# Performance work log

Hardware: AMD Instinct MI355X
Metric: run time of the kernel (lower is better)

The kernel has to match this reference:

```python
import jax, jax.numpy as jnp
import numpy as np

B, N, D_MODEL, H, BLK = 2, 2048, 1024, 16, 128
TB = N // BLK  # 16 blocks per side
NEG = -1e30


def setup_inputs() -> dict:
    key = jax.random.key(0)
    kq, kk, kv, kb = jax.random.split(key, 4)
    q = jax.random.normal(kq, (B, N, D_MODEL), jnp.float32)
    k = jax.random.normal(kk, (B, N, D_MODEL), jnp.float32)
    v = jax.random.normal(kv, (B, N, D_MODEL), jnp.float32)
    tau = jnp.float32(1.0)
    mask = jnp.ones((B, 1, N, N), jnp.int32)
    block_sparse_mask = jax.random.randint(kb, (TB, TB), 0, 2).astype(jnp.int32)
    return {"q": q, "k": k, "v": v, "tau": tau, "mask": mask,
            "block_sparse_mask": block_sparse_mask}


def reference(q, k, v, tau, mask, block_sparse_mask):
    # Equivalent closed form of the tiled online-softmax loop (dropout p=0, eval
    # mode): processed blocks accumulate exactly masked softmax(tau*QK^T/sqrt(dk))@V;
    # rows whose every block is skipped keep O=0, l=0, m=-inf.
    Bq, Nq, D = q.shape
    d_k = D // H
    qh = q.reshape(Bq, Nq, H, d_k).transpose(0, 2, 1, 3)  # (B,H,N,dk)
    kh = k.reshape(Bq, Nq, H, d_k).transpose(0, 2, 1, 3)
    vh = v.reshape(Bq, Nq, H, d_k).transpose(0, 2, 1, 3)

    S = tau * jnp.einsum('bhqd,bhkd->bhqk', qh, kh) / np.sqrt(d_k).astype(np.float32)

    # expand block-sparse pattern to token resolution (N,N)
    bs = jnp.repeat(jnp.repeat(block_sparse_mask, BLK, axis=0), BLK, axis=1)
    allowed = (mask != 0) & (bs != 0)  # (B,1,N,N), broadcasts over heads

    S_m = jnp.where(allowed, S, NEG)
    m = jnp.max(S_m, axis=-1, keepdims=True)            # (B,H,N,1)
    P = jnp.exp(S_m - m) * allowed.astype(S.dtype)      # masked exp-weights
    l = jnp.sum(P, axis=-1, keepdims=True)              # (B,H,N,1)
    Ov = jnp.einsum('bhqk,bhkd->bhqd', P, vh)
    O = Ov / jnp.where(l > 0, l, 1.0)

    has_any = jnp.any(allowed, axis=-1, keepdims=True)  # (B,1,N,1)
    m_out = jnp.where(has_any, m, -jnp.inf)
    O_out = O.transpose(0, 2, 1, 3).reshape(Bq, Nq, D)
    return O_out, l, m_out
```

## Files before the change

### kernel.cpp

```cpp
#include <hip/hip_runtime.h>
#include <hip/hip_bf16.h>

#define B_   2
#define N_   2048
#define DM_  1024
#define H_   16
#define DK_  64
#define BLK_ 128
#define TB_  16

typedef unsigned short u16;
typedef unsigned int   u32;
using bf16x8 = __attribute__((ext_vector_type(8))) __bf16;
using f32x4  = __attribute__((ext_vector_type(4))) float;

#define KPAD 72
#define VPAD 136
#define PPAD 136
#define OPAD 68
#define QROWS 64

__device__ __forceinline__ u32 pack_bf16(float a, float b) {
  __hip_bfloat162 h = __float22bfloat162_rn(make_float2(a, b));
  u32 u; __builtin_memcpy(&u, &h, 4); return u;
}
__device__ __forceinline__ bf16x8 pack8(float4 f0, float4 f1, float sc) {
  u32 w[4];
  w[0] = pack_bf16(f0.x * sc, f0.y * sc); w[1] = pack_bf16(f0.z * sc, f0.w * sc);
  w[2] = pack_bf16(f1.x * sc, f1.y * sc); w[3] = pack_bf16(f1.z * sc, f1.w * sc);
  bf16x8 r; __builtin_memcpy(&r, w, 16); return r;
}

__global__ void kv_convert(const float* __restrict__ k, const float* __restrict__ v,
                           u16* __restrict__ kb, u16* __restrict__ vt) {
  __shared__ u16 tile[BLK_][DK_ + 2];
  const int b = blockIdx.z, h = blockIdx.y, nb = blockIdx.x;
  const int t = threadIdx.x;
  const int rr = t >> 4, cc = (t & 15) * 4;
  {
    const float* kg = k + ((size_t)(b * N_ + nb * BLK_)) * DM_ + h * DK_;
    u16* kd = kb + ((size_t)((b * H_ + h) * N_) + nb * BLK_) * DK_;
#pragma unroll
    for (int i = 0; i < 8; ++i) {
      const int r = rr + i * 16;
      const float4 f = *(const float4*)(kg + (size_t)r * DM_ + cc);
      *(uint2*)(kd + r * DK_ + cc) = make_uint2(pack_bf16(f.x, f.y), pack_bf16(f.z, f.w));
    }
  }
  {
    const float* vg = v + ((size_t)(b * N_ + nb * BLK_)) * DM_ + h * DK_;
#pragma unroll
    for (int i = 0; i < 8; ++i) {
      const int r = rr + i * 16;
      const float4 f = *(const float4*)(vg + (size_t)r * DM_ + cc);
      *(u32*)(&tile[r][cc])     = pack_bf16(f.x, f.y);
      *(u32*)(&tile[r][cc + 2]) = pack_bf16(f.z, f.w);
    }
    __syncthreads();
    const int d = t & 63, n0 = (t >> 6) * 32;
    u16* og = vt + ((size_t)(b * H_ + h) * DK_ + d) * N_ + nb * BLK_ + n0;
#pragma unroll
    for (int j = 0; j < 32; j += 8) {
      u16 tmp[8];
#pragma unroll
      for (int x = 0; x < 8; ++x) tmp[x] = tile[n0 + j + x][d];
      uint4 w; __builtin_memcpy(&w, tmp, 16);
      *(uint4*)(og + j) = w;
    }
  }
}

__global__ void mask_flags_kernel(const int* __restrict__ mask, const int* __restrict__ bs,
                                  int* __restrict__ flags) {
  const int blk = blockIdx.x;
  const int kb = blk % TB_, qb = (blk / TB_) % TB_, b = blk / (TB_ * TB_);
  const int t = threadIdx.x;
  const int* mg = mask + (size_t)b * N_ * N_ + (size_t)(qb * BLK_) * N_ + kb * BLK_;
  int all1 = 1, any1 = 0;
  for (int i = t; i < BLK_ * BLK_ / 4; i += 256) {
    const int r = i >> 5, c = (i & 31) * 4;
    const int4 mv = *(const int4*)(mg + (size_t)r * N_ + c);
    all1 &= (mv.x != 0) & (mv.y != 0) & (mv.z != 0) & (mv.w != 0);
    any1 |= (mv.x != 0) | (mv.y != 0) | (mv.z != 0) | (mv.w != 0);
  }
  __shared__ int sAll[4], sAny[4];
  const int wv = t >> 6;
  const int wAll = __all(all1), wAny = __any(any1);
  if ((t & 63) == 0) { sAll[wv] = wAll; sAny[wv] = wAny; }
  __syncthreads();
  if (t == 0) {
    const int A = sAll[0] & sAll[1] & sAll[2] & sAll[3];
    const int O = sAny[0] | sAny[1] | sAny[2] | sAny[3];
    int f = 0;
    if (bs[qb * TB_ + kb] != 0 && O) f = A ? 1 : 2;
    flags[blk] = f;
  }
}

__global__ __launch_bounds__(256, 3)
void attn_kernel(const float* __restrict__ q_, const u16* __restrict__ kb_,
                 const u16* __restrict__ vt, const float* __restrict__ tau_p,
                 const int* __restrict__ mask, const int* __restrict__ flags,
                 float* __restrict__ o_out, float* __restrict__ l_out,
                 float* __restrict__ m_out) {
  __shared__ __align__(16) u16 lds[BLK_ * KPAD + DK_ * VPAD + QROWS * PPAD];
  u16* Ks  = lds;
  u16* Vts = Ks + BLK_ * KPAD;
  u16* Ps  = Vts + DK_ * VPAD;
  float* Os = (float*)lds;

  const int idx = blockIdx.x;
  const int bh = idx & 31, qb64 = idx >> 5;
  const int b = bh >> 4, h = bh & 15;
  const int qb128 = qb64 >> 1;
  const int t = threadIdx.x;
  const int wave = t >> 6, lane = t & 63, quad = lane >> 4, col = lane & 15;

  const int* flg = flags + (b * TB_ + qb128) * TB_;
  u32 actmask = 0, mixmask = 0;
#pragma unroll
  for (int i = 0; i < TB_; ++i) {
    const int f = flg[i];
    actmask |= (f != 0) ? (1u << i) : 0u;
    mixmask |= (f == 2) ? (1u << i) : 0u;
  }

  const int qg = qb64 * QROWS + wave * 16 + col;

  const float qscale = tau_p[0] * 0.125f * 1.44269504f;
  bf16x8 bq[2];
  {
    const float* qr = q_ + ((size_t)(b * N_ + qg)) * DM_ + h * DK_;
#pragma unroll
    for (int half = 0; half < 2; ++half) {
      const float4 f0 = *(const float4*)(qr + half * 32 + quad * 8);
      const float4 f1 = *(const float4*)(qr + half * 32 + quad * 8 + 4);
      bq[half] = pack8(f0, f1, qscale);
    }
  }

  float m_run  = -INFINITY;
  float m_true = -INFINITY;
  float l_run  = 0.f;
  f32x4 oacc[4];
#pragma unroll
  for (int mt = 0; mt < 4; ++mt) oacc[mt] = (f32x4){0.f, 0.f, 0.f, 0.f};

  const u16* kbase = kb_ + (size_t)(b * H_ + h) * N_ * DK_;
  const u16* vbase = vt + (size_t)(b * H_ + h) * DK_ * N_;

  u32 rem = actmask;
  while (rem) {
    const int cur = (int)__builtin_ctz(rem);
    rem &= rem - 1;
    const int mix = (mixmask >> cur) & 1;

    __syncthreads();
    {
      const u16* ks = kbase + (size_t)cur * BLK_ * DK_;
      const u16* vs = vbase + cur * BLK_;
      uint4 kr[4], vr[4];
#pragma unroll
      for (int j = 0; j < 4; ++j) {
        const int i = t + 256 * j;
        kr[j] = *(const uint4*)(ks + i * 8);
        vr[j] = *(const uint4*)(vs + (size_t)(i >> 4) * N_ + (i & 15) * 8);
      }
#pragma unroll
      for (int j = 0; j < 4; ++j) {
        const int i = t + 256 * j;
        *(uint4*)(Ks + (i >> 3) * KPAD + (i & 7) * 8) = kr[j];
        *(uint4*)(Vts + (i >> 4) * VPAD + (i & 15) * 8) = vr[j];
      }
    }
    __syncthreads();

    f32x4 st[8];
    __builtin_amdgcn_s_setprio(1);
#pragma unroll
    for (int kt = 0; kt < 8; ++kt) {
      const bf16x8 a0 = *(const bf16x8*)(Ks + (kt * 16 + col) * KPAD + quad * 8);
      const bf16x8 a1 = *(const bf16x8*)(Ks + (kt * 16 + col) * KPAD + 32 + quad * 8);
      f32x4 c = (f32x4){0.f, 0.f, 0.f, 0.f};
      c = __builtin_amdgcn_mfma_f32_16x16x32_bf16(a0, bq[0], c, 0, 0, 0);
      c = __builtin_amdgcn_mfma_f32_16x16x32_bf16(a1, bq[1], c, 0, 0, 0);
      st[kt] = c;
    }
    __builtin_amdgcn_s_setprio(0);
    if (mix) {
      const int* mg = mask + (size_t)b * N_ * N_ + (size_t)qg * N_ + cur * BLK_;
#pragma unroll
      for (int kt = 0; kt < 8; ++kt) {
        const int4 mv = *(const int4*)(mg + kt * 16 + quad * 4);
        if (!mv.x) st[kt][0] = -1e30f;
        if (!mv.y) st[kt][1] = -1e30f;
        if (!mv.z) st[kt][2] = -1e30f;
        if (!mv.w) st[kt][3] = -1e30f;
      }
    }
    float mx = -INFINITY;
#pragma unroll
    for (int kt = 0; kt < 8; ++kt)
      mx = fmaxf(mx, fmaxf(fmaxf(st[kt][0], st[kt][1]), fmaxf(st[kt][2], st[kt][3])));
    mx = fmaxf(mx, __shfl_xor(mx, 16, 64));
    mx = fmaxf(mx, __shfl_xor(mx, 32, 64));
    m_true = fmaxf(m_true, mx);

    const float mold = m_run;
    float mnew = mold;
    if (!__all(mx <= mold + 8.f)) {
      mnew = fmaxf(mold, mx);
      const float alpha = __builtin_amdgcn_exp2f(mold - mnew);
      l_run *= alpha;
#pragma unroll
      for (int mt = 0; mt < 4; ++mt)
#pragma unroll
        for (int r = 0; r < 4; ++r) oacc[mt][r] *= alpha;
      m_run = mnew;
    }

    const int qloc = wave * 16 + col;
    float s = 0.f;
    if (!mix) {
#pragma unroll
      for (int kt = 0; kt < 8; ++kt) {
        const float p0 = __builtin_amdgcn_exp2f(st[kt][0] - mnew);
        const float p1 = __builtin_amdgcn_exp2f(st[kt][1] - mnew);
        const float p2 = __builtin_amdgcn_exp2f(st[kt][2] - mnew);
        const float p3 = __builtin_amdgcn_exp2f(st[kt][3] - mnew);
        s += (p0 + p1) + (p2 + p3);
        *(uint2*)(Ps + qloc * PPAD + kt * 16 + quad * 4) =
            make_uint2(pack_bf16(p0, p1), pack_bf16(p2, p3));
      }
    } else {
#pragma unroll
      for (int kt = 0; kt < 8; ++kt) {
        const float p0 = st[kt][0] <= -1e29f ? 0.f : __builtin_amdgcn_exp2f(st[kt][0] - mnew);
        const float p1 = st[kt][1] <= -1e29f ? 0.f : __builtin_amdgcn_exp2f(st[kt][1] - mnew);
        const float p2 = st[kt][2] <= -1e29f ? 0.f : __builtin_amdgcn_exp2f(st[kt][2] - mnew);
        const float p3 = st[kt][3] <= -1e29f ? 0.f : __builtin_amdgcn_exp2f(st[kt][3] - mnew);
        s += (p0 + p1) + (p2 + p3);
        *(uint2*)(Ps + qloc * PPAD + kt * 16 + quad * 4) =
            make_uint2(pack_bf16(p0, p1), pack_bf16(p2, p3));
      }
    }
    s += __shfl_xor(s, 16, 64);
    s += __shfl_xor(s, 32, 64);
    l_run += s;

    __builtin_amdgcn_s_setprio(1);
#pragma unroll
    for (int ks = 0; ks < 4; ++ks) {
      const bf16x8 bfrag = *(const bf16x8*)(Ps + qloc * PPAD + ks * 32 + quad * 8);
#pragma unroll
      for (int mt = 0; mt < 4; ++mt) {
        const bf16x8 av = *(const bf16x8*)(Vts + (mt * 16 + col) * VPAD + ks * 32 + quad * 8);
        oacc[mt] = __builtin_amdgcn_mfma_f32_16x16x32_bf16(av, bfrag, oacc[mt], 0, 0, 0);
      }
    }
    __builtin_amdgcn_s_setprio(0);
  }

  __syncthreads();
  {
    const float inv = l_run > 0.f ? 1.f / l_run : 1.f;
    const int qloc = wave * 16 + col;
#pragma unroll
    for (int mt = 0; mt < 4; ++mt) {
      float4 w = make_float4(oacc[mt][0] * inv, oacc[mt][1] * inv,
                             oacc[mt][2] * inv, oacc[mt][3] * inv);
      *(float4*)(Os + qloc * OPAD + mt * 16 + quad * 4) = w;
    }
  }
  __syncthreads();
  float* ob = o_out + ((size_t)(b * N_ + qb64 * QROWS)) * DM_ + h * DK_;
#pragma unroll
  for (int j = 0; j < 4; ++j) {
    const int i = t + 256 * j;
    const int r = i >> 4, c4 = (i & 15) * 4;
    const float4 w = *(const float4*)(Os + r * OPAD + c4);
    *(float4*)(ob + (size_t)r * DM_ + c4) = w;
  }
  if (quad == 0) {
    const size_t oi = (size_t)(b * H_ + h) * N_ + qg;
    const float lv = l_run > 0.f
        ? l_run * __builtin_amdgcn_exp2f(m_run - m_true) : 0.f;
    l_out[oi] = lv;
    m_out[oi] = l_run > 0.f ? m_true * 0.69314718056f : -INFINITY;
  }
}

extern "C" void kernel_launch(void* const* d_in, const int* in_sizes, int n_in,
                              void* d_out, int out_size, void* d_ws, size_t ws_size,
                              hipStream_t stream) {
  const float* q   = (const float*)d_in[0];
  const float* k   = (const float*)d_in[1];
  const float* v   = (const float*)d_in[2];
  const float* tau = (const float*)d_in[3];
  const int* mask  = (const int*)d_in[4];
  const int* bs    = (const int*)d_in[5];
  float* out = (float*)d_out;

  const size_t plane = (size_t)B_ * H_ * N_ * DK_;
  u16* kb = (u16*)d_ws;
  u16* vt = kb + plane;
  int* flags = (int*)(vt + plane);

  kv_convert<<<dim3(N_ / BLK_, H_, B_), 256, 0, stream>>>(k, v, kb, vt);
  mask_flags_kernel<<<B_ * TB_ * TB_, 256, 0, stream>>>(mask, bs, flags);

  float* o_out = out;
  float* l_out = out + (size_t)B_ * N_ * DM_;
  float* m_out = l_out + (size_t)B_ * H_ * N_;
  attn_kernel<<<dim3((N_ / QROWS) * 32), 256, 0, stream>>>(q, kb, vt, tau, mask, flags,
                                                           o_out, l_out, m_out);
}
```

Baseline: 167.2 us.

## Stage K/V tiles via global_load_lds with pre-swizzled contiguous block images

The K/V conversion kernel now writes each 128-row block as a contiguous 8192-element image with an XOR swizzle on 16-byte chunks. The attention kernel then copies these images straight into LDS with global_load_lds, skipping the register round trip and padded stores. Fragment reads use matching XOR addressing in place of padding to avoid bank conflicts, which also shrinks LDS use. Loads are still synchronous with barriers, so no prefetch overlap is added.

```diff
diff --git a/kernel.cpp b/kernel.cpp
--- a/kernel.cpp
+++ b/kernel.cpp
@@ -14,8 +14,6 @@
 using bf16x8 = __attribute__((ext_vector_type(8))) __bf16;
 using f32x4  = __attribute__((ext_vector_type(4))) float;
 
-#define KPAD 72
-#define VPAD 136
 #define PPAD 136
 #define OPAD 68
 #define QROWS 64
@@ -32,19 +30,21 @@
 }
 
 __global__ void kv_convert(const float* __restrict__ k, const float* __restrict__ v,
-                           u16* __restrict__ kb, u16* __restrict__ vt) {
+                           u16* __restrict__ kimg, u16* __restrict__ vimg) {
   __shared__ u16 tile[BLK_][DK_ + 2];
   const int b = blockIdx.z, h = blockIdx.y, nb = blockIdx.x;
   const int t = threadIdx.x;
+  const size_t obase = ((size_t)((b * H_ + h) * TB_ + nb)) * 8192;
   const int rr = t >> 4, cc = (t & 15) * 4;
   {
     const float* kg = k + ((size_t)(b * N_ + nb * BLK_)) * DM_ + h * DK_;
-    u16* kd = kb + ((size_t)((b * H_ + h) * N_) + nb * BLK_) * DK_;
+    u16* kd = kimg + obase;
 #pragma unroll
     for (int i = 0; i < 8; ++i) {
       const int r = rr + i * 16;
       const float4 f = *(const float4*)(kg + (size_t)r * DM_ + cc);
-      *(uint2*)(kd + r * DK_ + cc) = make_uint2(pack_bf16(f.x, f.y), pack_bf16(f.z, f.w));
+      const int so = ((((cc >> 3) ^ (r & 7)) << 3) | (cc & 4));
+      *(uint2*)(kd + r * 64 + so) = make_uint2(pack_bf16(f.x, f.y), pack_bf16(f.z, f.w));
     }
   }
   {
@@ -58,14 +58,15 @@
     }
     __syncthreads();
     const int d = t & 63, n0 = (t >> 6) * 32;
-    u16* og = vt + ((size_t)(b * H_ + h) * DK_ + d) * N_ + nb * BLK_ + n0;
+    u16* og = vimg + obase + d * 128;
 #pragma unroll
     for (int j = 0; j < 32; j += 8) {
       u16 tmp[8];
 #pragma unroll
       for (int x = 0; x < 8; ++x) tmp[x] = tile[n0 + j + x][d];
       uint4 w; __builtin_memcpy(&w, tmp, 16);
-      *(uint4*)(og + j) = w;
+      const int chunk = (n0 + j) >> 3;
+      *(uint4*)(og + ((chunk ^ (d & 7)) << 3)) = w;
     }
   }
 }
@@ -97,16 +98,30 @@
   }
 }
 
+#define STAGE(blk_) do {                                                             \
+    const u16* ksrc_ = kpl + (size_t)(blk_) * 8192 + wave * 2048 + lane * 8;         \
+    const u16* vsrc_ = vpl + (size_t)(blk_) * 8192 + wave * 2048 + lane * 8;         \
+    u16* kdst_ = lds + wave * 2048;                                                  \
+    u16* vdst_ = lds + 8192 + wave * 2048;                                           \
+    _Pragma("unroll")                                                                \
+    for (int i2_ = 0; i2_ < 4; ++i2_) {                                              \
+      __builtin_amdgcn_global_load_lds(                                              \
+          (const __attribute__((address_space(1))) void*)(ksrc_ + i2_ * 512),        \
+          (__attribute__((address_space(3))) void*)(kdst_ + i2_ * 512), 16, 0, 0);   \
+      __builtin_amdgcn_global_load_lds(                                              \
+          (const __attribute__((address_space(1))) void*)(vsrc_ + i2_ * 512),        \
+          (__attribute__((address_space(3))) void*)(vdst_ + i2_ * 512), 16, 0, 0);   \
+    }                                                                                \
+  } while (0)
+
 __global__ __launch_bounds__(256, 3)
-void attn_kernel(const float* __restrict__ q_, const u16* __restrict__ kb_,
-                 const u16* __restrict__ vt, const float* __restrict__ tau_p,
+void attn_kernel(const float* __restrict__ q_, const u16* __restrict__ kimg,
+                 const u16* __restrict__ vimg, const float* __restrict__ tau_p,
                  const int* __restrict__ mask, const int* __restrict__ flags,
                  float* __restrict__ o_out, float* __restrict__ l_out,
                  float* __restrict__ m_out) {
-  __shared__ __align__(16) u16 lds[BLK_ * KPAD + DK_ * VPAD + QROWS * PPAD];
-  u16* Ks  = lds;
-  u16* Vts = Ks + BLK_ * KPAD;
-  u16* Ps  = Vts + DK_ * VPAD;
+  __shared__ __align__(16) u16 lds[8192 + 8192 + QROWS * PPAD];
+  u16* Ps  = lds + 16384;
   float* Os = (float*)lds;
 
   const int idx = blockIdx.x;
@@ -125,6 +140,9 @@
     mixmask |= (f == 2) ? (1u << i) : 0u;
   }
 
+  const u16* kpl = kimg + (size_t)(b * H_ + h) * TB_ * 8192;
+  const u16* vpl = vimg + (size_t)(b * H_ + h) * TB_ * 8192;
+
   const int qg = qb64 * QROWS + wave * 16 + col;
 
   const float qscale = tau_p[0] * 0.125f * 1.44269504f;
@@ -146,8 +164,9 @@
 #pragma unroll
   for (int mt = 0; mt < 4; ++mt) oacc[mt] = (f32x4){0.f, 0.f, 0.f, 0.f};
 
-  const u16* kbase = kb_ + (size_t)(b * H_ + h) * N_ * DK_;
-  const u16* vbase = vt + (size_t)(b * H_ + h) * DK_ * N_;
+  const int s8 = col & 7;
+  const int a0o = (quad ^ s8) << 3;
+  const int qloc = wave * 16 + col;
 
   u32 rem = actmask;
   while (rem) {
@@ -156,31 +175,16 @@
     const int mix = (mixmask >> cur) & 1;
 
     __syncthreads();
-    {
-      const u16* ks = kbase + (size_t)cur * BLK_ * DK_;
-      const u16* vs = vbase + cur * BLK_;
-      uint4 kr[4], vr[4];
-#pragma unroll
-      for (int j = 0; j < 4; ++j) {
-        const int i = t + 256 * j;
-        kr[j] = *(const uint4*)(ks + i * 8);
-        vr[j] = *(const uint4*)(vs + (size_t)(i >> 4) * N_ + (i & 15) * 8);
-      }
-#pragma unroll
-      for (int j = 0; j < 4; ++j) {
-        const int i = t + 256 * j;
-        *(uint4*)(Ks + (i >> 3) * KPAD + (i & 7) * 8) = kr[j];
-        *(uint4*)(Vts + (i >> 4) * VPAD + (i & 15) * 8) = vr[j];
-      }
-    }
+    STAGE(cur);
     __syncthreads();
 
     f32x4 st[8];
     __builtin_amdgcn_s_setprio(1);
 #pragma unroll
     for (int kt = 0; kt < 8; ++kt) {
-      const bf16x8 a0 = *(const bf16x8*)(Ks + (kt * 16 + col) * KPAD + quad * 8);
-      const bf16x8 a1 = *(const bf16x8*)(Ks + (kt * 16 + col) * KPAD + 32 + quad * 8);
+      const u16* krow = lds + (kt * 16 + col) * 64;
+      const bf16x8 a0 = *(const bf16x8*)(krow + a0o);
+      const bf16x8 a1 = *(const bf16x8*)(krow + (a0o ^ 32));
       f32x4 c = (f32x4){0.f, 0.f, 0.f, 0.f};
       c = __builtin_amdgcn_mfma_f32_16x16x32_bf16(a0, bq[0], c, 0, 0, 0);
       c = __builtin_amdgcn_mfma_f32_16x16x32_bf16(a1, bq[1], c, 0, 0, 0);
@@ -219,7 +223,6 @@
       m_run = mnew;
     }
 
-    const int qloc = wave * 16 + col;
     float s = 0.f;
     if (!mix) {
 #pragma unroll
@@ -254,7 +257,8 @@
       const bf16x8 bfrag = *(const bf16x8*)(Ps + qloc * PPAD + ks * 32 + quad * 8);
 #pragma unroll
       for (int mt = 0; mt < 4; ++mt) {
-        const bf16x8 av = *(const bf16x8*)(Vts + (mt * 16 + col) * VPAD + ks * 32 + quad * 8);
+        const bf16x8 av =
+            *(const bf16x8*)(lds + 8192 + (mt * 16 + col) * 128 + (((ks * 4 + quad) ^ s8) << 3));
         oacc[mt] = __builtin_amdgcn_mfma_f32_16x16x32_bf16(av, bfrag, oacc[mt], 0, 0, 0);
       }
     }
@@ -264,7 +268,6 @@
   __syncthreads();
   {
     const float inv = l_run > 0.f ? 1.f / l_run : 1.f;
-    const int qloc = wave * 16 + col;
 #pragma unroll
     for (int mt = 0; mt < 4; ++mt) {
       float4 w = make_float4(oacc[mt][0] * inv, oacc[mt][1] * inv,
@@ -302,16 +305,16 @@
   float* out = (float*)d_out;
 
   const size_t plane = (size_t)B_ * H_ * N_ * DK_;
-  u16* kb = (u16*)d_ws;
-  u16* vt = kb + plane;
-  int* flags = (int*)(vt + plane);
-
-  kv_convert<<<dim3(N_ / BLK_, H_, B_), 256, 0, stream>>>(k, v, kb, vt);
+  u16* kimg = (u16*)d_ws;
+  u16* vimg = kimg + plane;
+  int* flags = (int*)(vimg + plane);
+
+  kv_convert<<<dim3(TB_, H_, B_), 256, 0, stream>>>(k, v, kimg, vimg);
   mask_flags_kernel<<<B_ * TB_ * TB_, 256, 0, stream>>>(mask, bs, flags);
 
   float* o_out = out;
   float* l_out = out + (size_t)B_ * N_ * DM_;
   float* m_out = l_out + (size_t)B_ * H_ * N_;
-  attn_kernel<<<dim3((N_ / QROWS) * 32), 256, 0, stream>>>(q, kb, vt, tau, mask, flags,
+  attn_kernel<<<dim3((N_ / QROWS) * 32), 256, 0, stream>>>(q, kimg, vimg, tau, mask, flags,
                                                            o_out, l_out, m_out);
 }
```

New measurement: 165.9 us. No clear change (-0.8%).
